# Kernel optimization log

Hardware: AMD Instinct MI355X
Metric: run time of the kernel (lower is better)

## Reference

```python
import jax, jax.numpy as jnp
import numpy as np

HIDDEN = 128
POOL = 64
G = 4            # grid_size
NBHD = 2.0       # neighborhood_size (meters)
NUM_SCENES = 256
PEDS = 64        # pedestrians per scene (uniform seq_start_end)


def setup_inputs() -> dict:
    key = jax.random.key(0)
    k1, k2, k3 = jax.random.split(key, 3)
    hidden_states = jax.random.normal(k1, (NUM_SCENES * PEDS, HIDDEN), jnp.float32)
    positions = jax.random.uniform(k2, (NUM_SCENES * PEDS, 2), jnp.float32)
    fan_in = HIDDEN * G * G
    weight = jax.random.normal(k3, (fan_in, POOL), jnp.float32) / np.sqrt(fan_in)
    bias = jnp.zeros((POOL,), jnp.float32)
    return {
        "hidden_states": hidden_states,
        "positions": positions,
        "weight": weight,
        "bias": bias,
        "peds_per_scene": PEDS,
    }


def reference(hidden_states, positions, weight, bias, peds_per_scene):
    total, H = hidden_states.shape
    P = peds_per_scene
    B = total // P
    h = hidden_states.reshape(B, P, H)
    p = positions.reshape(B, P, 2)

    # rel[b, i, j] = pos[j] - pos[i]  (matches curr_pos - curr_pos[i:i+1])
    rel = p[:, None, :, :] - p[:, :, None, :]            # [B, P, P, 2]
    in_range = (jnp.abs(rel[..., 0]) <= NBHD) & (jnp.abs(rel[..., 1]) <= NBHD)
    not_self = ~jnp.eye(P, dtype=bool)[None]
    mask = in_range & not_self                            # [B, P, P]

    # int() truncation == floor here since (rel + NBHD) >= 0 inside the range check
    scale = G / (2.0 * NBHD)
    gx = jnp.clip(jnp.floor((rel[..., 0] + NBHD) * scale).astype(jnp.int32), 0, G - 1)
    gy = jnp.clip(jnp.floor((rel[..., 1] + NBHD) * scale).astype(jnp.int32), 0, G - 1)
    grid_idx = gy * G + gx                                # [B, P, P]

    # scatter-add of neighbor hidden states into G*G bins via masked one-hot
    onehot = jax.nn.one_hot(grid_idx, G * G, dtype=h.dtype) * mask[..., None].astype(h.dtype)
    grid = jnp.einsum('bijg,bjh->bigh', onehot, h)        # [B, P, G*G, H]

    flat = grid.reshape(B * P, G * G * H)                 # row-major: (grid_idx, hidden)
    return flat @ weight + bias                            # [total_peds, POOL]
```

## Files before the change

### kernel.cpp

```cpp
#include <hip/hip_runtime.h>
#include <cstdint>

#define PEDS   64
#define HIDDEN 128
#define POOL   64
#define GRIDG  4
#define NBHD   2.0f

typedef unsigned short u16;
typedef unsigned int   u32;
typedef __attribute__((ext_vector_type(8))) short bf16x8;
typedef __attribute__((ext_vector_type(4))) float f32x4;

__device__ __forceinline__ u16 f2bf(float f) {
    u32 u = __float_as_uint(f);
    u += 0x7fffu + ((u >> 16) & 1u);
    return (u16)(u >> 16);
}
__device__ __forceinline__ u32 pack2bf(float a, float b) {
    return (u32)f2bf(a) | ((u32)f2bf(b) << 16);
}

__global__ __launch_bounds__(512) void social_fused(
    const float* __restrict__ h, const float* __restrict__ pos,
    const float* __restrict__ w, const float* __restrict__ bias,
    float* __restrict__ out)
{
    __shared__ unsigned char LB[65536];
    unsigned char* gidx  = LB;
    u32*           wmask = (u32*)(LB + 4096);
    u16*           hA    = (u16*)(LB + 8192);
    u16*           hwT   = (u16*)(LB + 57344);

    const int s    = blockIdx.x;
    const int tid  = threadIdx.x;
    const int wv   = tid >> 6;
    const int lane = tid & 63;
    const int l15  = lane & 15;
    const int q    = lane >> 4;
    const int mt   = wv & 3;
    const int nh   = wv >> 2;

    float2 pp = ((const float2*)pos)[(size_t)s * PEDS + lane];
    float px = pp.x, py = pp.y;

    const int hrow = tid >> 3, hc = tid & 7;
    const float4* hsrc = (const float4*)(h + ((size_t)s * PEDS + hrow) * HIDDEN + hc * 16);
    float4 hv0 = hsrc[0], hv1 = hsrc[1], hv2 = hsrc[2], hv3 = hsrc[3];

    const int gi  = wv * 8 + (lane >> 3);
    const int gj0 = (lane & 7) * 8;
    const float pxi = __shfl(px, gi), pyi = __shfl(py, gi);
    u32 gpk0 = 0, gpk1 = 0, um = 0;
    const float scale = (float)GRIDG / (2.0f * NBHD);
#pragma unroll
    for (int u8 = 0; u8 < 8; ++u8) {
        int j = gj0 + u8;
        float rx = __shfl(px, j) - pxi;
        float ry = __shfl(py, j) - pyi;
        u32 gb = 0xffu;
        if ((gi != j) && (fabsf(rx) <= NBHD) && (fabsf(ry) <= NBHD)) {
            int gx = (int)floorf((rx + NBHD) * scale); gx = min(max(gx, 0), GRIDG - 1);
            int gy = (int)floorf((ry + NBHD) * scale); gy = min(max(gy, 0), GRIDG - 1);
            int g = gy * GRIDG + gx;
            gb = (u32)g; um |= 1u << g;
        }
        if (u8 < 4) gpk0 |= gb << (u8 * 8); else gpk1 |= gb << ((u8 - 4) * 8);
    }
    *(uint2*)&gidx[gi * 64 + gj0] = make_uint2(gpk0, gpk1);

#pragma unroll
    for (int off = 32; off; off >>= 1) um |= __shfl_xor(um, off);
    if (lane == 0) wmask[wv] = um;

    {
        u32 p0 = pack2bf(hv0.x, hv0.y), p1 = pack2bf(hv0.z, hv0.w);
        u32 p2 = pack2bf(hv1.x, hv1.y), p3 = pack2bf(hv1.z, hv1.w);
        int ch = hc * 2;
        *(uint4*)&hA[hrow * 128 + ((ch ^ (hrow & 15)) << 3)] = make_uint4(p0, p1, p2, p3);
        p0 = pack2bf(hv2.x, hv2.y); p1 = pack2bf(hv2.z, hv2.w);
        p2 = pack2bf(hv3.x, hv3.y); p3 = pack2bf(hv3.z, hv3.w);
        ch = hc * 2 + 1;
        *(uint4*)&hA[hrow * 128 + ((ch ^ (hrow & 15)) << 3)] = make_uint4(p0, p1, p2, p3);
    }
    __syncthreads();

    u32 mask = wmask[0] | wmask[1] | wmask[2] | wmask[3]
             | wmask[4] | wmask[5] | wmask[6] | wmask[7];
    mask = __builtin_amdgcn_readfirstlane(mask);

    bf16x8 af[4];
#pragma unroll
    for (int st4 = 0; st4 < 4; ++st4)
        af[st4] = *(const bf16x8*)&hA[(mt * 16 + l15) * 128 + (((st4 * 4 + q) ^ l15) << 3)];

    const int ng = __popc(mask);
    u32 rem = mask;
    int g = 0;
    if (rem) { g = __ffs(rem) - 1; rem &= rem - 1u; }

    float wr[16];
    const int wc = lane, wk = wv * 16;
    if (ng) {
        const float* wsrc = w + ((size_t)g * HIDDEN + wk) * POOL + wc;
#pragma unroll
        for (int e = 0; e < 16; ++e) wr[e] = wsrc[(size_t)e * POOL];
    }

    f32x4 oacc[2];
    oacc[0] = (f32x4){0.f, 0.f, 0.f, 0.f};
    oacc[1] = (f32x4){0.f, 0.f, 0.f, 0.f};

    for (int t = 0; t < ng; ++t) {
        u16* wSb = (u16*)(LB + 24576 + ((t & 1) << 14));
#pragma unroll
        for (int cc = 0; cc < 2; ++cc) {
            u32 p0 = pack2bf(wr[cc * 8 + 0], wr[cc * 8 + 1]);
            u32 p1 = pack2bf(wr[cc * 8 + 2], wr[cc * 8 + 3]);
            u32 p2 = pack2bf(wr[cc * 8 + 4], wr[cc * 8 + 5]);
            u32 p3 = pack2bf(wr[cc * 8 + 6], wr[cc * 8 + 7]);
            int ch = wv * 2 + cc;
            *(uint4*)&wSb[wc * 128 + ((ch ^ (wc & 15)) << 3)] = make_uint4(p0, p1, p2, p3);
        }
        int gn = -1;
        if (rem) { gn = __ffs(rem) - 1; rem &= rem - 1u; }
        if (gn >= 0) {
            const float* wsrc = w + ((size_t)gn * HIDDEN + wk) * POOL + wc;
#pragma unroll
            for (int e = 0; e < 16; ++e) wr[e] = wsrc[(size_t)e * POOL];
        }
        __syncthreads();

        f32x4 a1[2];
        a1[0] = (f32x4){0.f, 0.f, 0.f, 0.f};
        a1[1] = (f32x4){0.f, 0.f, 0.f, 0.f};
#pragma unroll
        for (int st4 = 0; st4 < 4; ++st4) {
            int chs = ((st4 * 4 + q) ^ l15) << 3;
            bf16x8 b0 = *(const bf16x8*)&wSb[(nh * 32 + l15) * 128 + chs];
            bf16x8 b1 = *(const bf16x8*)&wSb[(nh * 32 + 16 + l15) * 128 + chs];
            a1[0] = __builtin_amdgcn_mfma_f32_16x16x32_bf16(af[st4], b0, a1[0], 0, 0, 0);
            a1[1] = __builtin_amdgcn_mfma_f32_16x16x32_bf16(af[st4], b1, a1[1], 0, 0, 0);
        }
#pragma unroll
        for (int ni = 0; ni < 2; ++ni) {
            int c = nh * 32 + ni * 16 + l15;
            u32 lo = pack2bf(a1[ni][0], a1[ni][1]);
            u32 hi = pack2bf(a1[ni][2], a1[ni][3]);
            *(uint2*)&hwT[c * 64 + (((mt * 4 + q) ^ (c & 15)) << 2)] = make_uint2(lo, hi);
        }
        __syncthreads();

#pragma unroll
        for (int kk = 0; kk < 2; ++kk) {
            uint2 gg = *(const uint2*)&gidx[(mt * 16 + l15) * 64 + kk * 32 + q * 8];
            union { u16 hx[8]; bf16x8 v; } mu;
#pragma unroll
            for (int b = 0; b < 4; ++b)
                mu.hx[b]     = (((gg.x >> (b * 8)) & 0xffu) == (u32)g) ? (u16)0x3F80 : (u16)0;
#pragma unroll
            for (int b = 0; b < 4; ++b)
                mu.hx[4 + b] = (((gg.y >> (b * 8)) & 0xffu) == (u32)g) ? (u16)0x3F80 : (u16)0;
#pragma unroll
            for (int ni = 0; ni < 2; ++ni) {
                int c = nh * 32 + ni * 16 + l15;
                int cs = c & 15;
                uint2 b0 = *(const uint2*)&hwT[c * 64 + (((kk * 8 + q * 2 + 0) ^ cs) << 2)];
                uint2 b1 = *(const uint2*)&hwT[c * 64 + (((kk * 8 + q * 2 + 1) ^ cs) << 2)];
                union { u32 u[4]; bf16x8 v; } bu;
                bu.u[0] = b0.x; bu.u[1] = b0.y; bu.u[2] = b1.x; bu.u[3] = b1.y;
                oacc[ni] = __builtin_amdgcn_mfma_f32_16x16x32_bf16(mu.v, bu.v, oacc[ni], 0, 0, 0);
            }
        }
        g = gn;
    }

#pragma unroll
    for (int ni = 0; ni < 2; ++ni) {
        int c = nh * 32 + ni * 16 + l15;
        float bv = bias[c];
        size_t ob = ((size_t)s * PEDS + mt * 16 + q * 4) * POOL + c;
#pragma unroll
        for (int r = 0; r < 4; ++r)
            out[ob + (size_t)r * POOL] = oacc[ni][r] + bv;
    }
}

extern "C" void kernel_launch(void* const* d_in, const int* in_sizes, int n_in,
                              void* d_out, int out_size, void* d_ws, size_t ws_size,
                              hipStream_t stream) {
    const float* h    = (const float*)d_in[0];
    const float* pos  = (const float*)d_in[1];
    const float* w    = (const float*)d_in[2];
    const float* bias = (const float*)d_in[3];
    float* out = (float*)d_out;

    const int total = in_sizes[0] / HIDDEN;
    const int B     = total / PEDS;

    hipLaunchKernelGGL(social_fused, dim3(B), dim3(512), 0, stream,
                       h, pos, w, bias, out);
}
```

Measured before the change: 70.43 us.

## Split into bf16 prepack kernel and main kernel with fragment-layout operands

A new prep kernel converts hidden states and weights to bf16 once, storing them in the MFMA fragment layout in workspace. The main kernel can then load A and B fragments straight from global memory with no per-block LDS staging and no per-block conversion of the full weight matrix. The main kernel now runs two blocks of 256 threads per scene, each owning half the output columns. It processes four grid cells per batch to cut barriers, and it keeps the per-row grid indices in registers rather than in LDS. The cost is an extra launch plus a write and re-read of the bf16 copies through workspace.

```diff
diff --git a/kernel.cpp b/kernel.cpp
--- a/kernel.cpp
+++ b/kernel.cpp
@@ -21,168 +21,164 @@
     return (u32)f2bf(a) | ((u32)f2bf(b) << 16);
 }
 
-__global__ __launch_bounds__(512) void social_fused(
-    const float* __restrict__ h, const float* __restrict__ pos,
-    const float* __restrict__ w, const float* __restrict__ bias,
+__global__ __launch_bounds__(256) void prep_kernel(
+    const float* __restrict__ h, const float* __restrict__ w,
+    u16* __restrict__ hB, u16* __restrict__ wB, int hb_threads)
+{
+    int t = blockIdx.x * 256 + threadIdx.x;
+    if (t < hb_threads) {
+        int lane = t & 63, st4 = (t >> 6) & 3, mt = (t >> 8) & 3, scene = t >> 10;
+        int row = scene * 64 + mt * 16 + (lane & 15);
+        int k0  = st4 * 32 + (lane >> 4) * 8;
+        const float4* s = (const float4*)(h + (size_t)row * HIDDEN + k0);
+        float4 f0 = s[0], f1 = s[1];
+        *(uint4*)(hB + (size_t)t * 8) = make_uint4(
+            pack2bf(f0.x, f0.y), pack2bf(f0.z, f0.w),
+            pack2bf(f1.x, f1.y), pack2bf(f1.z, f1.w));
+    } else {
+        int u = t - hb_threads;
+        if (u < 16 * 4 * 4 * 64) {
+            int lane = u & 63, st4 = (u >> 6) & 3, cg = (u >> 8) & 3, g = u >> 10;
+            int c  = cg * 16 + (lane & 15);
+            int k0 = st4 * 32 + (lane >> 4) * 8;
+            const float* s = w + ((size_t)g * HIDDEN + k0) * POOL + c;
+            float v[8];
+#pragma unroll
+            for (int e = 0; e < 8; ++e) v[e] = s[(size_t)e * POOL];
+            *(uint4*)(wB + (size_t)u * 8) = make_uint4(
+                pack2bf(v[0], v[1]), pack2bf(v[2], v[3]),
+                pack2bf(v[4], v[5]), pack2bf(v[6], v[7]));
+        }
+    }
+}
+
+__global__ __launch_bounds__(256) void social_main(
+    const u16* __restrict__ hB, const u16* __restrict__ wB,
+    const float* __restrict__ pos, const float* __restrict__ bias,
     float* __restrict__ out)
 {
-    __shared__ unsigned char LB[65536];
-    unsigned char* gidx  = LB;
-    u32*           wmask = (u32*)(LB + 4096);
-    u16*           hA    = (u16*)(LB + 8192);
-    u16*           hwT   = (u16*)(LB + 57344);
-
-    const int s    = blockIdx.x;
+    __shared__ u32 wmask[4];
+    __shared__ u16 hwT[32 * 256];
+
     const int tid  = threadIdx.x;
-    const int wv   = tid >> 6;
+    const int mt   = tid >> 6;
     const int lane = tid & 63;
     const int l15  = lane & 15;
     const int q    = lane >> 4;
-    const int mt   = wv & 3;
-    const int nh   = wv >> 2;
-
-    float2 pp = ((const float2*)pos)[(size_t)s * PEDS + lane];
-    float px = pp.x, py = pp.y;
-
-    const int hrow = tid >> 3, hc = tid & 7;
-    const float4* hsrc = (const float4*)(h + ((size_t)s * PEDS + hrow) * HIDDEN + hc * 16);
-    float4 hv0 = hsrc[0], hv1 = hsrc[1], hv2 = hsrc[2], hv3 = hsrc[3];
-
-    const int gi  = wv * 8 + (lane >> 3);
-    const int gj0 = (lane & 7) * 8;
-    const float pxi = __shfl(px, gi), pyi = __shfl(py, gi);
-    u32 gpk0 = 0, gpk1 = 0, um = 0;
+    const int scene = blockIdx.x >> 1;
+    const int ch    = blockIdx.x & 1;
+
+    bf16x8 af[4];
+    const u16* hfb = hB + (((size_t)scene * 4 + mt) * 4) * 512;
+#pragma unroll
+    for (int st4 = 0; st4 < 4; ++st4)
+        af[st4] = *(const bf16x8*)(hfb + st4 * 512 + lane * 8);
+
+    const float bv0 = bias[ch * 32 + l15];
+    const float bv1 = bias[ch * 32 + 16 + l15];
+
+    float2 pp = ((const float2*)pos)[(size_t)scene * PEDS + lane];
+    const int i = mt * 16 + l15;
+    const float pxi = __shfl(pp.x, i), pyi = __shfl(pp.y, i);
     const float scale = (float)GRIDG / (2.0f * NBHD);
-#pragma unroll
-    for (int u8 = 0; u8 < 8; ++u8) {
-        int j = gj0 + u8;
-        float rx = __shfl(px, j) - pxi;
-        float ry = __shfl(py, j) - pyi;
-        u32 gb = 0xffu;
-        if ((gi != j) && (fabsf(rx) <= NBHD) && (fabsf(ry) <= NBHD)) {
-            int gx = (int)floorf((rx + NBHD) * scale); gx = min(max(gx, 0), GRIDG - 1);
-            int gy = (int)floorf((ry + NBHD) * scale); gy = min(max(gy, 0), GRIDG - 1);
-            int g = gy * GRIDG + gx;
-            gb = (u32)g; um |= 1u << g;
-        }
-        if (u8 < 4) gpk0 |= gb << (u8 * 8); else gpk1 |= gb << ((u8 - 4) * 8);
-    }
-    *(uint2*)&gidx[gi * 64 + gj0] = make_uint2(gpk0, gpk1);
-
+    u32 gpk[4] = {0u, 0u, 0u, 0u};
+    u32 um = 0u;
+#pragma unroll
+    for (int jh = 0; jh < 2; ++jh) {
+#pragma unroll
+        for (int u8 = 0; u8 < 8; ++u8) {
+            int j = jh * 32 + q * 8 + u8;
+            float rx = __shfl(pp.x, j) - pxi;
+            float ry = __shfl(pp.y, j) - pyi;
+            u32 gb = 0xffu;
+            if ((i != j) && (fabsf(rx) <= NBHD) && (fabsf(ry) <= NBHD)) {
+                int gx = (int)floorf((rx + NBHD) * scale); gx = min(max(gx, 0), GRIDG - 1);
+                int gy = (int)floorf((ry + NBHD) * scale); gy = min(max(gy, 0), GRIDG - 1);
+                gb = (u32)(gy * GRIDG + gx);
+                um |= 1u << gb;
+            }
+            gpk[jh * 2 + (u8 >> 2)] |= gb << ((u8 & 3) * 8);
+        }
+    }
 #pragma unroll
     for (int off = 32; off; off >>= 1) um |= __shfl_xor(um, off);
-    if (lane == 0) wmask[wv] = um;
-
-    {
-        u32 p0 = pack2bf(hv0.x, hv0.y), p1 = pack2bf(hv0.z, hv0.w);
-        u32 p2 = pack2bf(hv1.x, hv1.y), p3 = pack2bf(hv1.z, hv1.w);
-        int ch = hc * 2;
-        *(uint4*)&hA[hrow * 128 + ((ch ^ (hrow & 15)) << 3)] = make_uint4(p0, p1, p2, p3);
-        p0 = pack2bf(hv2.x, hv2.y); p1 = pack2bf(hv2.z, hv2.w);
-        p2 = pack2bf(hv3.x, hv3.y); p3 = pack2bf(hv3.z, hv3.w);
-        ch = hc * 2 + 1;
-        *(uint4*)&hA[hrow * 128 + ((ch ^ (hrow & 15)) << 3)] = make_uint4(p0, p1, p2, p3);
-    }
+    if (lane == 0) wmask[mt] = um;
     __syncthreads();
 
-    u32 mask = wmask[0] | wmask[1] | wmask[2] | wmask[3]
-             | wmask[4] | wmask[5] | wmask[6] | wmask[7];
+    u32 mask = wmask[0] | wmask[1] | wmask[2] | wmask[3];
     mask = __builtin_amdgcn_readfirstlane(mask);
 
-    bf16x8 af[4];
-#pragma unroll
-    for (int st4 = 0; st4 < 4; ++st4)
-        af[st4] = *(const bf16x8*)&hA[(mt * 16 + l15) * 128 + (((st4 * 4 + q) ^ l15) << 3)];
-
-    const int ng = __popc(mask);
+    f32x4 oacc0 = (f32x4){0.f, 0.f, 0.f, 0.f};
+    f32x4 oacc1 = (f32x4){0.f, 0.f, 0.f, 0.f};
     u32 rem = mask;
-    int g = 0;
-    if (rem) { g = __ffs(rem) - 1; rem &= rem - 1u; }
-
-    float wr[16];
-    const int wc = lane, wk = wv * 16;
-    if (ng) {
-        const float* wsrc = w + ((size_t)g * HIDDEN + wk) * POOL + wc;
-#pragma unroll
-        for (int e = 0; e < 16; ++e) wr[e] = wsrc[(size_t)e * POOL];
-    }
-
-    f32x4 oacc[2];
-    oacc[0] = (f32x4){0.f, 0.f, 0.f, 0.f};
-    oacc[1] = (f32x4){0.f, 0.f, 0.f, 0.f};
-
-    for (int t = 0; t < ng; ++t) {
-        u16* wSb = (u16*)(LB + 24576 + ((t & 1) << 14));
-#pragma unroll
-        for (int cc = 0; cc < 2; ++cc) {
-            u32 p0 = pack2bf(wr[cc * 8 + 0], wr[cc * 8 + 1]);
-            u32 p1 = pack2bf(wr[cc * 8 + 2], wr[cc * 8 + 3]);
-            u32 p2 = pack2bf(wr[cc * 8 + 4], wr[cc * 8 + 5]);
-            u32 p3 = pack2bf(wr[cc * 8 + 6], wr[cc * 8 + 7]);
-            int ch = wv * 2 + cc;
-            *(uint4*)&wSb[wc * 128 + ((ch ^ (wc & 15)) << 3)] = make_uint4(p0, p1, p2, p3);
-        }
-        int gn = -1;
-        if (rem) { gn = __ffs(rem) - 1; rem &= rem - 1u; }
-        if (gn >= 0) {
-            const float* wsrc = w + ((size_t)gn * HIDDEN + wk) * POOL + wc;
-#pragma unroll
-            for (int e = 0; e < 16; ++e) wr[e] = wsrc[(size_t)e * POOL];
+
+    while (true) {
+        int gs[4];
+#pragma unroll
+        for (int t = 0; t < 4; ++t) {
+            gs[t] = rem ? (__ffs(rem) - 1) : -1;
+            if (rem) rem &= rem - 1u;
+        }
+
+#pragma unroll
+        for (int t = 0; t < 4; ++t) {
+            int ge = gs[t] < 0 ? 0 : gs[t];
+            const u16* wf0 = wB + (((size_t)ge * 4 + ch * 2 + 0) * 4) * 512;
+            const u16* wf1 = wB + (((size_t)ge * 4 + ch * 2 + 1) * 4) * 512;
+            f32x4 a10 = (f32x4){0.f, 0.f, 0.f, 0.f};
+            f32x4 a11 = (f32x4){0.f, 0.f, 0.f, 0.f};
+#pragma unroll
+            for (int st4 = 0; st4 < 4; ++st4) {
+                bf16x8 b0 = *(const bf16x8*)(wf0 + st4 * 512 + lane * 8);
+                bf16x8 b1 = *(const bf16x8*)(wf1 + st4 * 512 + lane * 8);
+                a10 = __builtin_amdgcn_mfma_f32_16x16x32_bf16(af[st4], b0, a10, 0, 0, 0);
+                a11 = __builtin_amdgcn_mfma_f32_16x16x32_bf16(af[st4], b1, a11, 0, 0, 0);
+            }
+            int ci = t * 8 + mt * 2 + (q >> 1);
+#pragma unroll
+            for (int ni = 0; ni < 2; ++ni) {
+                const f32x4& a = ni ? a11 : a10;
+                int cr  = ni * 16 + l15;
+                int ci2 = (ci & 0x10) | ((ci & 15) ^ l15);
+                *(uint2*)&hwT[cr * 256 + ci2 * 8 + (q & 1) * 4] =
+                    make_uint2(pack2bf(a[0], a[1]), pack2bf(a[2], a[3]));
+            }
         }
         __syncthreads();
 
-        f32x4 a1[2];
-        a1[0] = (f32x4){0.f, 0.f, 0.f, 0.f};
-        a1[1] = (f32x4){0.f, 0.f, 0.f, 0.f};
-#pragma unroll
-        for (int st4 = 0; st4 < 4; ++st4) {
-            int chs = ((st4 * 4 + q) ^ l15) << 3;
-            bf16x8 b0 = *(const bf16x8*)&wSb[(nh * 32 + l15) * 128 + chs];
-            bf16x8 b1 = *(const bf16x8*)&wSb[(nh * 32 + 16 + l15) * 128 + chs];
-            a1[0] = __builtin_amdgcn_mfma_f32_16x16x32_bf16(af[st4], b0, a1[0], 0, 0, 0);
-            a1[1] = __builtin_amdgcn_mfma_f32_16x16x32_bf16(af[st4], b1, a1[1], 0, 0, 0);
-        }
-#pragma unroll
-        for (int ni = 0; ni < 2; ++ni) {
-            int c = nh * 32 + ni * 16 + l15;
-            u32 lo = pack2bf(a1[ni][0], a1[ni][1]);
-            u32 hi = pack2bf(a1[ni][2], a1[ni][3]);
-            *(uint2*)&hwT[c * 64 + (((mt * 4 + q) ^ (c & 15)) << 2)] = make_uint2(lo, hi);
-        }
+#pragma unroll
+        for (int step = 0; step < 8; ++step) {
+            int slot = step >> 1, jh = step & 1;
+            int gt = gs[slot];
+            u32 wa = gpk[jh * 2], wb = gpk[jh * 2 + 1];
+            union { u16 hx[8]; bf16x8 v; } mu;
+#pragma unroll
+            for (int b = 0; b < 4; ++b)
+                mu.hx[b]     = (((wa >> (b * 8)) & 0xffu) == (u32)gt) ? (u16)0x3F80 : (u16)0;
+#pragma unroll
+            for (int b = 0; b < 4; ++b)
+                mu.hx[4 + b] = (((wb >> (b * 8)) & 0xffu) == (u32)gt) ? (u16)0x3F80 : (u16)0;
+            int ci = step * 4 + q;
+#pragma unroll
+            for (int ni = 0; ni < 2; ++ni) {
+                int cr  = ni * 16 + l15;
+                int ci2 = (ci & 0x10) | ((ci & 15) ^ l15);
+                bf16x8 bb = *(const bf16x8*)&hwT[cr * 256 + ci2 * 8];
+                if (ni == 0)
+                    oacc0 = __builtin_amdgcn_mfma_f32_16x16x32_bf16(mu.v, bb, oacc0, 0, 0, 0);
+                else
+                    oacc1 = __builtin_amdgcn_mfma_f32_16x16x32_bf16(mu.v, bb, oacc1, 0, 0, 0);
+            }
+        }
+        if (!rem) break;
         __syncthreads();
-
-#pragma unroll
-        for (int kk = 0; kk < 2; ++kk) {
-            uint2 gg = *(const uint2*)&gidx[(mt * 16 + l15) * 64 + kk * 32 + q * 8];
-            union { u16 hx[8]; bf16x8 v; } mu;
-#pragma unroll
-            for (int b = 0; b < 4; ++b)
-                mu.hx[b]     = (((gg.x >> (b * 8)) & 0xffu) == (u32)g) ? (u16)0x3F80 : (u16)0;
-#pragma unroll
-            for (int b = 0; b < 4; ++b)
-                mu.hx[4 + b] = (((gg.y >> (b * 8)) & 0xffu) == (u32)g) ? (u16)0x3F80 : (u16)0;
-#pragma unroll
-            for (int ni = 0; ni < 2; ++ni) {
-                int c = nh * 32 + ni * 16 + l15;
-                int cs = c & 15;
-                uint2 b0 = *(const uint2*)&hwT[c * 64 + (((kk * 8 + q * 2 + 0) ^ cs) << 2)];
-                uint2 b1 = *(const uint2*)&hwT[c * 64 + (((kk * 8 + q * 2 + 1) ^ cs) << 2)];
-                union { u32 u[4]; bf16x8 v; } bu;
-                bu.u[0] = b0.x; bu.u[1] = b0.y; bu.u[2] = b1.x; bu.u[3] = b1.y;
-                oacc[ni] = __builtin_amdgcn_mfma_f32_16x16x32_bf16(mu.v, bu.v, oacc[ni], 0, 0, 0);
-            }
-        }
-        g = gn;
-    }
-
-#pragma unroll
-    for (int ni = 0; ni < 2; ++ni) {
-        int c = nh * 32 + ni * 16 + l15;
-        float bv = bias[c];
-        size_t ob = ((size_t)s * PEDS + mt * 16 + q * 4) * POOL + c;
-#pragma unroll
-        for (int r = 0; r < 4; ++r)
-            out[ob + (size_t)r * POOL] = oacc[ni][r] + bv;
+    }
+
+    size_t ob = ((size_t)scene * PEDS + mt * 16 + q * 4) * POOL + ch * 32 + l15;
+#pragma unroll
+    for (int r = 0; r < 4; ++r) {
+        out[ob + (size_t)r * POOL]      = oacc0[r] + bv0;
+        out[ob + (size_t)r * POOL + 16] = oacc1[r] + bv1;
     }
 }
 
@@ -198,6 +194,15 @@
     const int total = in_sizes[0] / HIDDEN;
     const int B     = total / PEDS;
 
-    hipLaunchKernelGGL(social_fused, dim3(B), dim3(512), 0, stream,
-                       h, pos, w, bias, out);
-}
+    u16* hB = (u16*)d_ws;
+    u16* wB = hB + (size_t)total * HIDDEN;
+
+    const int hb_threads = total * 16;
+    const int wb_threads = 16 * 4 * 4 * 64;
+    const int prep_blocks = (hb_threads + wb_threads + 255) / 256;
+
+    hipLaunchKernelGGL(prep_kernel, dim3(prep_blocks), dim3(256), 0, stream,
+                       h, w, hB, wB, hb_threads);
+    hipLaunchKernelGGL(social_main, dim3(B * 2), dim3(256), 0, stream,
+                       hB, wB, pos, bias, out);
+}
```

Measured after the change: 75.20 us. 6.8% more time.
